# Performance work log

Hardware: AMD Instinct MI355X
Metric: run time of the kernel (lower is better)

Reference implementation:

```python
import jax, jax.numpy as jnp
import numpy as np

N_NODES = 50000
N_EDGES = 1200000
BATCH = 64
D_IN = 2
D_EMB = 64
EPS = 1e-12


def _l2norm(x):
    # torch.nn.functional.normalize(dim=1): x / max(||x||_2, eps)
    n = jnp.sqrt(jnp.sum(x * x, axis=1, keepdims=True))
    return x / jnp.maximum(n, EPS)


def setup_inputs() -> dict:
    key = jax.random.key(0)
    ks = jax.random.split(key, 10)
    edge_row = jnp.sort(jax.random.randint(ks[0], (N_EDGES,), 0, N_NODES, dtype=jnp.int32))
    edge_col = jax.random.randint(ks[1], (N_EDGES,), 0, N_NODES, dtype=jnp.int32)
    batch_assign = jax.random.randint(ks[2], (N_NODES,), 0, BATCH, dtype=jnp.int32)
    input_features = jax.random.uniform(ks[3], (N_NODES, D_IN), dtype=jnp.float32)
    input_feature_s = jax.random.uniform(ks[4], (BATCH, D_IN), dtype=jnp.float32)
    W1 = jax.random.normal(ks[5], (D_IN, D_EMB), dtype=jnp.float32) * 0.1
    W2 = jax.random.normal(ks[6], (D_EMB, D_EMB), dtype=jnp.float32) * 0.1
    W3 = jax.random.normal(ks[7], (D_EMB, D_EMB), dtype=jnp.float32) * 0.1
    Wl = jax.random.normal(ks[8], (2 * D_EMB, D_EMB), dtype=jnp.float32) * 0.1
    bl = jnp.zeros((D_EMB,), dtype=jnp.float32)
    return {
        "edge_row": edge_row, "edge_col": edge_col, "batch_assign": batch_assign,
        "input_features": input_features, "input_feature_s": input_feature_s,
        "W1": W1, "W2": W2, "W3": W3, "Wl": Wl, "bl": bl, "depth": 3,
    }


def reference(edge_row, edge_col, batch_assign, input_features, input_feature_s,
              W1, W2, W3, Wl, bl, depth):
    n_nodes = input_features.shape[0]
    n_batch = input_feature_s.shape[0]

    h = _l2norm(jax.nn.relu(input_features @ W1))        # [N, d]
    hs = _l2norm(jax.nn.relu(input_feature_s @ W1))      # [B, d]

    for _ in range(depth):
        # SPMM node_node @ h : gather neighbor embeddings, sum per destination row
        h_nv = jax.ops.segment_sum(h[edge_col], edge_row, num_segments=n_nodes)  # [N, d]
        # SPMM batch_node @ h : pool node embeddings per graph
        h_nv_s = jax.ops.segment_sum(h, batch_assign, num_segments=n_batch)      # [B, d]
        h = _l2norm(jax.nn.relu(jnp.concatenate([h @ W2, h_nv @ W3], axis=1) @ Wl + bl))
        hs = _l2norm(jax.nn.relu(jnp.concatenate([hs @ W2, h_nv_s @ W3], axis=1) @ Wl + bl))
    return (h, hs)
```

## Files before the change

kernel.cpp:

```cpp
#include <hip/hip_runtime.h>
#include <math.h>

#define N_NODES 50000
#define N_EDGES 1200000
#define BATCH   64
#define D       64
#define EPS     1e-12f
#define NCOPY   64
#define NODE_BLOCKS 3125
#define HS_BLOCKS   4
#define ITER_GRID  (NODE_BLOCKS + HS_BLOCKS)

__device__ __forceinline__ int rfl(int v) { return __builtin_amdgcn_readfirstlane(v); }

__global__ void __launch_bounds__(512) k_prep(const int* __restrict__ edge_row,
                                              int* __restrict__ row_start,
                                              float* __restrict__ pools,
                                              const float* __restrict__ W2,
                                              const float* __restrict__ W3,
                                              const float* __restrict__ Wl,
                                              float* __restrict__ MM4) {
    if (blockIdx.x < 98) {
        int tid = blockIdx.x * 512 + threadIdx.x;
        for (int i = tid; i < 2 * NCOPY * BATCH * D; i += 98 * 512) pools[i] = 0.f;
        if (tid > N_NODES) return;
        int lo = 0, hi = N_EDGES;
        while (lo < hi) {
            int mid = (lo + hi) >> 1;
            if (edge_row[mid] < tid) lo = mid + 1; else hi = mid;
        }
        row_start[tid] = lo;
    } else {
        for (int p = threadIdx.x; p < D * D; p += 512) {
            int k = p >> 6, j = p & 63;
            float a2 = 0.f, a3 = 0.f;
            for (int q = 0; q < D; ++q) {
                a2 += W2[k*D + q] * Wl[q*D + j];
                a3 += W3[k*D + q] * Wl[(D + q)*D + j];
            }
            MM4[(k >> 1) * D * 4 + j * 4 + (k & 1) * 2 + 0] = a2;
            MM4[(k >> 1) * D * 4 + j * 4 + (k & 1) * 2 + 1] = a3;
        }
    }
}

__device__ __forceinline__ float wave_l2norm(float v) {
    float ss = v * v;
    #pragma unroll
    for (int off = 32; off; off >>= 1) ss += __shfl_xor(ss, off);
    return ss;
}

__global__ void __launch_bounds__(256) k_init(const float* __restrict__ X,
                                              const float* __restrict__ Xs,
                                              const float* __restrict__ W1,
                                              float* __restrict__ B0,
                                              float* __restrict__ HS,
                                              const int* __restrict__ batch,
                                              float* __restrict__ P0) {
    int row = blockIdx.x * 4 + (threadIdx.x >> 6);
    int j   = threadIdx.x & 63;
    if (row >= N_NODES + BATCH) return;
    float x0, x1; float* out;
    bool is_node = (row < N_NODES);
    if (is_node) {
        x0 = X[row*2]; x1 = X[row*2 + 1]; out = B0 + (size_t)row * D;
    } else {
        int r = row - N_NODES;
        x0 = Xs[r*2]; x1 = Xs[r*2 + 1]; out = HS + (size_t)r * D;
    }
    float v = fmaxf(fmaf(x0, W1[j], x1 * W1[D + j]), 0.f);
    float n = sqrtf(wave_l2norm(v));
    float val = v / fmaxf(n, EPS);
    out[j] = val;
    if (is_node) {
        int b = rfl(batch[row]);
        atomicAdd(&P0[(blockIdx.x & (NCOPY - 1)) * (BATCH * D) + b * D + j], val);
    }
}

__global__ void __launch_bounds__(512, 8) k_iter(const int* __restrict__ edge_col,
                                                 const int* __restrict__ row_start,
                                                 const float* __restrict__ Hc,
                                                 float* __restrict__ Hn,
                                                 const float* __restrict__ MM4,
                                                 const float* __restrict__ bl,
                                                 const int* __restrict__ batch,
                                                 float* __restrict__ Pout,
                                                 float* __restrict__ HSrw,
                                                 float* __restrict__ Pin) {
    __shared__ float4 sMM[32 * 64];
    __shared__ float4 sHG[8 * 64];
    int t = threadIdx.x;
    const float4* gMM = (const float4*)MM4;
    for (int i = t; i < 32 * 64; i += 512) sMM[i] = gMM[i];
    __syncthreads();
    int w = t >> 6, l = t & 63;
    bool is_node = (blockIdx.x < NODE_BLOCKS);
    int rA, rB;
    float hvA, hvB, gvA, gvB;

    if (is_node) {
        int pr = blockIdx.x * 8 + w;
        rA = 2 * pr; rB = rA + 1;
        int sA = rfl(row_start[rA]);
        int eA = rfl(row_start[rB]);
        int eB = rfl(row_start[rB + 1]);
        hvA = Hc[(size_t)rA * D + l];
        hvB = Hc[(size_t)rB * D + l];
        float aA = 0.f, aB = 0.f;
        int pad = 0;
        for (int base = sA; base < eB; ) {
            int cw = eB - base; if (cw > 64) cw = 64;
            int col = 0;
            if (l < cw) col = edge_col[base + l];
            int nb = (cw + 15) >> 4;
            pad += (nb << 4) - cw;
            for (int b = 0; b < nb; ++b) {
                #pragma unroll
                for (int u = 0; u < 16; ++u) {
                    int idx = (b << 4) + u;
                    int c = __builtin_amdgcn_readlane(col, idx);
                    const float* rp = Hc + (size_t)c * D;
                    float v = rp[l];
                    if (base + idx < eA) aA += v; else aB += v;
                }
            }
            base += cw;
        }
        aB -= (float)pad * Hc[l];
        gvA = aA; gvB = aB;
    } else {
        int pr = (blockIdx.x - NODE_BLOCKS) * 8 + w;
        rA = 2 * pr; rB = rA + 1;
        hvA = HSrw[(size_t)rA * D + l];
        hvB = HSrw[(size_t)rB * D + l];
        float aA = 0.f, aB = 0.f;
        #pragma unroll 4
        for (int c = 0; c < NCOPY; ++c) {
            float* pA = Pin + (size_t)c * (BATCH * D) + rA * D + l;
            float vA = pA[0], vB = pA[D];
            pA[0] = 0.f; pA[D] = 0.f;
            aA += vA; aB += vB;
        }
        gvA = aA; gvB = aB;
    }

    sHG[w * 64 + l] = make_float4(hvA, hvB, gvA, gvB);
    float biasl = bl[l];
    float a2x = 0.f, a2y = 0.f, a3x = biasl, a3y = biasl;
    const float4* hg = &sHG[w * 64];
    #pragma unroll
    for (int kk = 0; kk < 32; ++kk) {
        float4 mm = sMM[kk * 64 + l];
        float4 h0 = hg[2 * kk];
        float4 h1 = hg[2 * kk + 1];
        a2x = fmaf(h0.x, mm.x, a2x); a2y = fmaf(h0.y, mm.x, a2y);
        a3x = fmaf(h0.z, mm.y, a3x); a3y = fmaf(h0.w, mm.y, a3y);
        a2x = fmaf(h1.x, mm.z, a2x); a2y = fmaf(h1.y, mm.z, a2y);
        a3x = fmaf(h1.z, mm.w, a3x); a3y = fmaf(h1.w, mm.w, a3y);
    }
    float vA = fmaxf(a2x + a3x, 0.f);
    float vB = fmaxf(a2y + a3y, 0.f);
    float ssA = vA * vA, ssB = vB * vB;
    #pragma unroll
    for (int off = 32; off; off >>= 1) {
        ssA += __shfl_xor(ssA, off);
        ssB += __shfl_xor(ssB, off);
    }
    float oA = vA / fmaxf(sqrtf(ssA), EPS);
    float oB = vB / fmaxf(sqrtf(ssB), EPS);

    if (is_node) {
        Hn[(size_t)rA * D + l] = oA;
        Hn[(size_t)rB * D + l] = oB;
        if (Pout) {
            int bA = rfl(batch[rA]);
            int bB = rfl(batch[rB]);
            float* cp = Pout + (size_t)(blockIdx.x & (NCOPY - 1)) * (BATCH * D);
            atomicAdd(&cp[bA * D + l], oA);
            atomicAdd(&cp[bB * D + l], oB);
        }
    } else {
        HSrw[(size_t)rA * D + l] = oA;
        HSrw[(size_t)rB * D + l] = oB;
    }
}

extern "C" void kernel_launch(void* const* d_in, const int* in_sizes, int n_in,
                              void* d_out, int out_size, void* d_ws, size_t ws_size,
                              hipStream_t stream) {
    const int*   edge_row = (const int*)  d_in[0];
    const int*   edge_col = (const int*)  d_in[1];
    const int*   batch    = (const int*)  d_in[2];
    const float* X        = (const float*)d_in[3];
    const float* Xs       = (const float*)d_in[4];
    const float* W1       = (const float*)d_in[5];
    const float* W2       = (const float*)d_in[6];
    const float* W3       = (const float*)d_in[7];
    const float* Wl       = (const float*)d_in[8];
    const float* bl       = (const float*)d_in[9];

    float* H  = (float*)d_out;
    float* HS = (float*)d_out + (size_t)N_NODES * D;

    float* B0  = (float*)d_ws;
    float* B1  = B0 + (size_t)N_NODES * D;
    float* PA  = B1 + (size_t)N_NODES * D;
    float* PB  = PA + (size_t)NCOPY * BATCH * D;
    float* MM4 = PB + (size_t)NCOPY * BATCH * D;
    int*   row_start = (int*)(MM4 + 32 * 64 * 4);

    k_prep<<<99, 512, 0, stream>>>(edge_row, row_start, PA, W2, W3, Wl, MM4);
    k_init<<<(N_NODES + BATCH + 3) / 4, 256, 0, stream>>>(X, Xs, W1, B0, HS, batch, PA);

    k_iter<<<ITER_GRID, 512, 0, stream>>>(edge_col, row_start, B0, B1, MM4, bl, batch, PB, HS, PA);
    k_iter<<<ITER_GRID, 512, 0, stream>>>(edge_col, row_start, B1, B0, MM4, bl, batch, PA, HS, PB);
    k_iter<<<ITER_GRID, 512, 0, stream>>>(edge_col, row_start, B0, H, MM4, bl, batch, nullptr, HS, PA);
}
```

Before: 281.7 us.

## Fuse prologue kernels, process four rows per wave, and lag batch pooling by a layer

The edge-boundary, weight-product and initial-embedding kernels are merged into one prologue. Row starts are now found by scattering at edge-row boundaries instead of a binary search per node. Each wave in the iteration kernel now handles four destination rows rather than two, with per-edge bounds guards replacing the padding correction. Batch pooling now accumulates the input embedding of each layer, so the batch update runs one launch later and a small extra launch finishes the last one. This removes the separate init atomics and amortises edge-index loads and row-start reads over more rows, at the cost of more registers per thread (launch bounds lowered to 6) and one extra kernel launch.

```diff
diff --git a/kernel.cpp b/kernel.cpp
--- a/kernel.cpp
+++ b/kernel.cpp
@@ -7,79 +7,68 @@
 #define D       64
 #define EPS     1e-12f
 #define NCOPY   64
-#define NODE_BLOCKS 3125
-#define HS_BLOCKS   4
-#define ITER_GRID  (NODE_BLOCKS + HS_BLOCKS)
+#define PSZ     (NCOPY * BATCH * D)
+
+#define EB  2344
+#define MMB 8
+#define IB  6258
+#define NODE_BLOCKS 1563
+#define NW4 12500
 
 __device__ __forceinline__ int rfl(int v) { return __builtin_amdgcn_readfirstlane(v); }
 
-__global__ void __launch_bounds__(512) k_prep(const int* __restrict__ edge_row,
-                                              int* __restrict__ row_start,
-                                              float* __restrict__ pools,
-                                              const float* __restrict__ W2,
-                                              const float* __restrict__ W3,
-                                              const float* __restrict__ Wl,
-                                              float* __restrict__ MM4) {
-    if (blockIdx.x < 98) {
-        int tid = blockIdx.x * 512 + threadIdx.x;
-        for (int i = tid; i < 2 * NCOPY * BATCH * D; i += 98 * 512) pools[i] = 0.f;
-        if (tid > N_NODES) return;
-        int lo = 0, hi = N_EDGES;
-        while (lo < hi) {
-            int mid = (lo + hi) >> 1;
-            if (edge_row[mid] < tid) lo = mid + 1; else hi = mid;
-        }
-        row_start[tid] = lo;
+__global__ void __launch_bounds__(512) k_pro(const int* __restrict__ edge_row,
+                                             int* __restrict__ row_start,
+                                             float* __restrict__ PA, float* __restrict__ PB,
+                                             const float* __restrict__ W2,
+                                             const float* __restrict__ W3,
+                                             const float* __restrict__ Wl,
+                                             float* __restrict__ MM4,
+                                             const float* __restrict__ X,
+                                             const float* __restrict__ Xs,
+                                             const float* __restrict__ W1,
+                                             float* __restrict__ B0,
+                                             float* __restrict__ HS) {
+    int bid = blockIdx.x, t = threadIdx.x;
+    if (bid < EB) {
+        int tid = bid * 512 + t;
+        for (int i = tid; i < PSZ; i += EB * 512) { PA[i] = 0.f; PB[i] = 0.f; }
+        if (tid < N_EDGES) {
+            int b = edge_row[tid];
+            int a = (tid == 0) ? -1 : edge_row[tid - 1];
+            for (int r = a + 1; r <= b; ++r) row_start[r] = tid;
+            if (tid == N_EDGES - 1)
+                for (int r = b + 1; r <= N_NODES; ++r) row_start[r] = N_EDGES;
+        }
+    } else if (bid < EB + MMB) {
+        int k = (bid - EB) * 8 + (t >> 6), j = t & 63;
+        float a2 = 0.f, a3 = 0.f;
+        for (int q = 0; q < D; ++q) {
+            a2 += W2[k*D + q] * Wl[q*D + j];
+            a3 += W3[k*D + q] * Wl[(D + q)*D + j];
+        }
+        MM4[(k >> 1) * (D * 4) + j * 4 + (k & 1) * 2 + 0] = a2;
+        MM4[(k >> 1) * (D * 4) + j * 4 + (k & 1) * 2 + 1] = a3;
     } else {
-        for (int p = threadIdx.x; p < D * D; p += 512) {
-            int k = p >> 6, j = p & 63;
-            float a2 = 0.f, a3 = 0.f;
-            for (int q = 0; q < D; ++q) {
-                a2 += W2[k*D + q] * Wl[q*D + j];
-                a3 += W3[k*D + q] * Wl[(D + q)*D + j];
-            }
-            MM4[(k >> 1) * D * 4 + j * 4 + (k & 1) * 2 + 0] = a2;
-            MM4[(k >> 1) * D * 4 + j * 4 + (k & 1) * 2 + 1] = a3;
-        }
+        int row = (bid - EB - MMB) * 8 + (t >> 6);
+        int j = t & 63;
+        if (row >= N_NODES + BATCH) return;
+        float x0, x1; float* out;
+        if (row < N_NODES) {
+            x0 = X[row*2]; x1 = X[row*2 + 1]; out = B0 + (size_t)row * D;
+        } else {
+            int r = row - N_NODES;
+            x0 = Xs[r*2]; x1 = Xs[r*2 + 1]; out = HS + (size_t)r * D;
+        }
+        float v = fmaxf(fmaf(x0, W1[j], x1 * W1[D + j]), 0.f);
+        float ss = v * v;
+        #pragma unroll
+        for (int off = 32; off; off >>= 1) ss += __shfl_xor(ss, off);
+        out[j] = v / fmaxf(sqrtf(ss), EPS);
     }
 }
 
-__device__ __forceinline__ float wave_l2norm(float v) {
-    float ss = v * v;
-    #pragma unroll
-    for (int off = 32; off; off >>= 1) ss += __shfl_xor(ss, off);
-    return ss;
-}
-
-__global__ void __launch_bounds__(256) k_init(const float* __restrict__ X,
-                                              const float* __restrict__ Xs,
-                                              const float* __restrict__ W1,
-                                              float* __restrict__ B0,
-                                              float* __restrict__ HS,
-                                              const int* __restrict__ batch,
-                                              float* __restrict__ P0) {
-    int row = blockIdx.x * 4 + (threadIdx.x >> 6);
-    int j   = threadIdx.x & 63;
-    if (row >= N_NODES + BATCH) return;
-    float x0, x1; float* out;
-    bool is_node = (row < N_NODES);
-    if (is_node) {
-        x0 = X[row*2]; x1 = X[row*2 + 1]; out = B0 + (size_t)row * D;
-    } else {
-        int r = row - N_NODES;
-        x0 = Xs[r*2]; x1 = Xs[r*2 + 1]; out = HS + (size_t)r * D;
-    }
-    float v = fmaxf(fmaf(x0, W1[j], x1 * W1[D + j]), 0.f);
-    float n = sqrtf(wave_l2norm(v));
-    float val = v / fmaxf(n, EPS);
-    out[j] = val;
-    if (is_node) {
-        int b = rfl(batch[row]);
-        atomicAdd(&P0[(blockIdx.x & (NCOPY - 1)) * (BATCH * D) + b * D + j], val);
-    }
-}
-
-__global__ void __launch_bounds__(512, 8) k_iter(const int* __restrict__ edge_col,
+__global__ void __launch_bounds__(512, 6) k_iter(const int* __restrict__ edge_col,
                                                  const int* __restrict__ row_start,
                                                  const float* __restrict__ Hc,
                                                  float* __restrict__ Hn,
@@ -88,103 +77,123 @@
                                                  const int* __restrict__ batch,
                                                  float* __restrict__ Pout,
                                                  float* __restrict__ HSrw,
-                                                 float* __restrict__ Pin) {
+                                                 float* __restrict__ Pin,
+                                                 int hs_blocks) {
     __shared__ float4 sMM[32 * 64];
-    __shared__ float4 sHG[8 * 64];
-    int t = threadIdx.x;
+    __shared__ float4 sH[8 * 64];
+    __shared__ float4 sG[8 * 64];
+    int t = threadIdx.x, w = t >> 6, l = t & 63;
     const float4* gMM = (const float4*)MM4;
-    for (int i = t; i < 32 * 64; i += 512) sMM[i] = gMM[i];
+    for (int i = t; i < 2048; i += 512) sMM[i] = gMM[i];
     __syncthreads();
-    int w = t >> 6, l = t & 63;
-    bool is_node = (blockIdx.x < NODE_BLOCKS);
-    int rA, rB;
-    float hvA, hvB, gvA, gvB;
-
-    if (is_node) {
-        int pr = blockIdx.x * 8 + w;
-        rA = 2 * pr; rB = rA + 1;
-        int sA = rfl(row_start[rA]);
-        int eA = rfl(row_start[rB]);
-        int eB = rfl(row_start[rB + 1]);
-        hvA = Hc[(size_t)rA * D + l];
-        hvB = Hc[(size_t)rB * D + l];
-        float aA = 0.f, aB = 0.f;
-        int pad = 0;
-        for (int base = sA; base < eB; ) {
-            int cw = eB - base; if (cw > 64) cw = 64;
+
+    int bid = blockIdx.x;
+    bool is_hs = (bid < hs_blocks);
+    float hv0, hv1, hv2, hv3, gv0, gv1, gv2, gv3;
+    int rbase;
+
+    if (!is_hs) {
+        int g4 = (bid - hs_blocks) * 8 + w;
+        if (g4 >= NW4) return;
+        rbase = g4 * 4;
+        int eS  = rfl(row_start[rbase]);
+        int eA  = rfl(row_start[rbase + 1]);
+        int eBb = rfl(row_start[rbase + 2]);
+        int eC  = rfl(row_start[rbase + 3]);
+        int eD_ = rfl(row_start[rbase + 4]);
+        hv0 = Hc[(size_t)(rbase + 0) * D + l];
+        hv1 = Hc[(size_t)(rbase + 1) * D + l];
+        hv2 = Hc[(size_t)(rbase + 2) * D + l];
+        hv3 = Hc[(size_t)(rbase + 3) * D + l];
+        float aA = 0.f, aB = 0.f, aC = 0.f, aD = 0.f;
+        for (int base = eS; base < eD_; base += 64) {
+            int cw = eD_ - base; if (cw > 64) cw = 64;
             int col = 0;
             if (l < cw) col = edge_col[base + l];
             int nb = (cw + 15) >> 4;
-            pad += (nb << 4) - cw;
             for (int b = 0; b < nb; ++b) {
                 #pragma unroll
                 for (int u = 0; u < 16; ++u) {
-                    int idx = (b << 4) + u;
-                    int c = __builtin_amdgcn_readlane(col, idx);
-                    const float* rp = Hc + (size_t)c * D;
-                    float v = rp[l];
-                    if (base + idx < eA) aA += v; else aB += v;
+                    int o = (b << 4) + u;
+                    int eidx = base + o;
+                    if (eidx < eD_) {
+                        int c = __builtin_amdgcn_readlane(col, o);
+                        float v = Hc[(size_t)c * D + l];
+                        if (eidx < eA)       aA += v;
+                        else if (eidx < eBb) aB += v;
+                        else if (eidx < eC)  aC += v;
+                        else                 aD += v;
+                    }
                 }
             }
-            base += cw;
-        }
-        aB -= (float)pad * Hc[l];
-        gvA = aA; gvB = aB;
+        }
+        gv0 = aA; gv1 = aB; gv2 = aC; gv3 = aD;
+        float* cp = Pout + (size_t)(bid & (NCOPY - 1)) * (BATCH * D);
+        int b0 = rfl(batch[rbase + 0]);
+        int b1 = rfl(batch[rbase + 1]);
+        int b2 = rfl(batch[rbase + 2]);
+        int b3 = rfl(batch[rbase + 3]);
+        atomicAdd(&cp[b0 * D + l], hv0);
+        atomicAdd(&cp[b1 * D + l], hv1);
+        atomicAdd(&cp[b2 * D + l], hv2);
+        atomicAdd(&cp[b3 * D + l], hv3);
     } else {
-        int pr = (blockIdx.x - NODE_BLOCKS) * 8 + w;
-        rA = 2 * pr; rB = rA + 1;
-        hvA = HSrw[(size_t)rA * D + l];
-        hvB = HSrw[(size_t)rB * D + l];
-        float aA = 0.f, aB = 0.f;
+        int g4 = bid * 8 + w;
+        if (g4 >= 16) return;
+        rbase = g4 * 4;
+        hv0 = HSrw[(size_t)(rbase + 0) * D + l];
+        hv1 = HSrw[(size_t)(rbase + 1) * D + l];
+        hv2 = HSrw[(size_t)(rbase + 2) * D + l];
+        hv3 = HSrw[(size_t)(rbase + 3) * D + l];
+        float aA = 0.f, aB = 0.f, aC = 0.f, aD = 0.f;
         #pragma unroll 4
         for (int c = 0; c < NCOPY; ++c) {
-            float* pA = Pin + (size_t)c * (BATCH * D) + rA * D + l;
-            float vA = pA[0], vB = pA[D];
-            pA[0] = 0.f; pA[D] = 0.f;
-            aA += vA; aB += vB;
-        }
-        gvA = aA; gvB = aB;
-    }
-
-    sHG[w * 64 + l] = make_float4(hvA, hvB, gvA, gvB);
-    float biasl = bl[l];
-    float a2x = 0.f, a2y = 0.f, a3x = biasl, a3y = biasl;
-    const float4* hg = &sHG[w * 64];
+            float* p = Pin + (size_t)c * (BATCH * D) + rbase * D + l;
+            float v0 = p[0], v1 = p[D], v2 = p[2*D], v3 = p[3*D];
+            p[0] = 0.f; p[D] = 0.f; p[2*D] = 0.f; p[3*D] = 0.f;
+            aA += v0; aB += v1; aC += v2; aD += v3;
+        }
+        gv0 = aA; gv1 = aB; gv2 = aC; gv3 = aD;
+    }
+
+    sH[w * 64 + l] = make_float4(hv0, hv1, hv2, hv3);
+    sG[w * 64 + l] = make_float4(gv0, gv1, gv2, gv3);
+    float bj = bl[l];
+    float a2A = 0.f, a2B = 0.f, a2C = 0.f, a2D = 0.f;
+    float a3A = bj,  a3B = bj,  a3C = bj,  a3D = bj;
+    const float4* ph = &sH[w * 64];
+    const float4* pg = &sG[w * 64];
     #pragma unroll
     for (int kk = 0; kk < 32; ++kk) {
         float4 mm = sMM[kk * 64 + l];
-        float4 h0 = hg[2 * kk];
-        float4 h1 = hg[2 * kk + 1];
-        a2x = fmaf(h0.x, mm.x, a2x); a2y = fmaf(h0.y, mm.x, a2y);
-        a3x = fmaf(h0.z, mm.y, a3x); a3y = fmaf(h0.w, mm.y, a3y);
-        a2x = fmaf(h1.x, mm.z, a2x); a2y = fmaf(h1.y, mm.z, a2y);
-        a3x = fmaf(h1.z, mm.w, a3x); a3y = fmaf(h1.w, mm.w, a3y);
-    }
-    float vA = fmaxf(a2x + a3x, 0.f);
-    float vB = fmaxf(a2y + a3y, 0.f);
-    float ssA = vA * vA, ssB = vB * vB;
+        float4 h0 = ph[2 * kk], h1 = ph[2 * kk + 1];
+        float4 g0 = pg[2 * kk], g1 = pg[2 * kk + 1];
+        a2A = fmaf(h0.x, mm.x, a2A); a2B = fmaf(h0.y, mm.x, a2B);
+        a2C = fmaf(h0.z, mm.x, a2C); a2D = fmaf(h0.w, mm.x, a2D);
+        a3A = fmaf(g0.x, mm.y, a3A); a3B = fmaf(g0.y, mm.y, a3B);
+        a3C = fmaf(g0.z, mm.y, a3C); a3D = fmaf(g0.w, mm.y, a3D);
+        a2A = fmaf(h1.x, mm.z, a2A); a2B = fmaf(h1.y, mm.z, a2B);
+        a2C = fmaf(h1.z, mm.z, a2C); a2D = fmaf(h1.w, mm.z, a2D);
+        a3A = fmaf(g1.x, mm.w, a3A); a3B = fmaf(g1.y, mm.w, a3B);
+        a3C = fmaf(g1.z, mm.w, a3C); a3D = fmaf(g1.w, mm.w, a3D);
+    }
+    float v0 = fmaxf(a2A + a3A, 0.f);
+    float v1 = fmaxf(a2B + a3B, 0.f);
+    float v2 = fmaxf(a2C + a3C, 0.f);
+    float v3 = fmaxf(a2D + a3D, 0.f);
+    float s0 = v0*v0, s1 = v1*v1, s2 = v2*v2, s3 = v3*v3;
     #pragma unroll
     for (int off = 32; off; off >>= 1) {
-        ssA += __shfl_xor(ssA, off);
-        ssB += __shfl_xor(ssB, off);
-    }
-    float oA = vA / fmaxf(sqrtf(ssA), EPS);
-    float oB = vB / fmaxf(sqrtf(ssB), EPS);
-
-    if (is_node) {
-        Hn[(size_t)rA * D + l] = oA;
-        Hn[(size_t)rB * D + l] = oB;
-        if (Pout) {
-            int bA = rfl(batch[rA]);
-            int bB = rfl(batch[rB]);
-            float* cp = Pout + (size_t)(blockIdx.x & (NCOPY - 1)) * (BATCH * D);
-            atomicAdd(&cp[bA * D + l], oA);
-            atomicAdd(&cp[bB * D + l], oB);
-        }
-    } else {
-        HSrw[(size_t)rA * D + l] = oA;
-        HSrw[(size_t)rB * D + l] = oB;
-    }
+        s0 += __shfl_xor(s0, off); s1 += __shfl_xor(s1, off);
+        s2 += __shfl_xor(s2, off); s3 += __shfl_xor(s3, off);
+    }
+    v0 /= fmaxf(sqrtf(s0), EPS); v1 /= fmaxf(sqrtf(s1), EPS);
+    v2 /= fmaxf(sqrtf(s2), EPS); v3 /= fmaxf(sqrtf(s3), EPS);
+    float* out = is_hs ? HSrw : Hn;
+    out[(size_t)(rbase + 0) * D + l] = v0;
+    out[(size_t)(rbase + 1) * D + l] = v1;
+    out[(size_t)(rbase + 2) * D + l] = v2;
+    out[(size_t)(rbase + 3) * D + l] = v3;
 }
 
 extern "C" void kernel_launch(void* const* d_in, const int* in_sizes, int n_in,
@@ -207,14 +216,19 @@
     float* B0  = (float*)d_ws;
     float* B1  = B0 + (size_t)N_NODES * D;
     float* PA  = B1 + (size_t)N_NODES * D;
-    float* PB  = PA + (size_t)NCOPY * BATCH * D;
-    float* MM4 = PB + (size_t)NCOPY * BATCH * D;
+    float* PB  = PA + PSZ;
+    float* MM4 = PB + PSZ;
     int*   row_start = (int*)(MM4 + 32 * 64 * 4);
 
-    k_prep<<<99, 512, 0, stream>>>(edge_row, row_start, PA, W2, W3, Wl, MM4);
-    k_init<<<(N_NODES + BATCH + 3) / 4, 256, 0, stream>>>(X, Xs, W1, B0, HS, batch, PA);
-
-    k_iter<<<ITER_GRID, 512, 0, stream>>>(edge_col, row_start, B0, B1, MM4, bl, batch, PB, HS, PA);
-    k_iter<<<ITER_GRID, 512, 0, stream>>>(edge_col, row_start, B1, B0, MM4, bl, batch, PA, HS, PB);
-    k_iter<<<ITER_GRID, 512, 0, stream>>>(edge_col, row_start, B0, H, MM4, bl, batch, nullptr, HS, PA);
+    k_pro<<<EB + MMB + IB, 512, 0, stream>>>(edge_row, row_start, PA, PB,
+                                             W2, W3, Wl, MM4, X, Xs, W1, B0, HS);
+
+    k_iter<<<NODE_BLOCKS, 512, 0, stream>>>(edge_col, row_start, B0, B1, MM4, bl,
+                                            batch, PA, HS, PA, 0);
+    k_iter<<<NODE_BLOCKS + 2, 512, 0, stream>>>(edge_col, row_start, B1, B0, MM4, bl,
+                                                batch, PB, HS, PA, 2);
+    k_iter<<<NODE_BLOCKS + 2, 512, 0, stream>>>(edge_col, row_start, B0, H, MM4, bl,
+                                                batch, PA, HS, PB, 2);
+    k_iter<<<2, 512, 0, stream>>>(edge_col, row_start, B0, B0, MM4, bl,
+                                  batch, PB, HS, PA, 2);
 }
```

Result: slower. 482.6 us (+71.3%).

## Fuse prep and init kernels, compute row_start per edge, pool inputs in iterations

Applied to the files above, without the earlier changes.

The separate prep and init kernels become one prologue kernel, and the row_start binary search is replaced by a per-edge boundary scan that writes row offsets directly. Batch pooling now happens in each iteration on the input embeddings rather than the outputs, which removes the atomics from init. The batch-embedding update therefore runs one launch later, and a small HS-only launch is added at the end. Launch count stays the same. The point is to remove the serial binary-search work and the standalone init atomics, at the cost of a more intricate buffer ping-pong schedule across launches.

```diff
diff --git a/kernel.cpp b/kernel.cpp
--- a/kernel.cpp
+++ b/kernel.cpp
@@ -7,75 +7,64 @@
 #define D       64
 #define EPS     1e-12f
 #define NCOPY   64
+#define PSZ     (NCOPY * BATCH * D)
+
+#define EB  2344
+#define MMB 8
+#define IB  6258
 #define NODE_BLOCKS 3125
-#define HS_BLOCKS   4
-#define ITER_GRID  (NODE_BLOCKS + HS_BLOCKS)
+#define HSB 4
 
 __device__ __forceinline__ int rfl(int v) { return __builtin_amdgcn_readfirstlane(v); }
 
-__global__ void __launch_bounds__(512) k_prep(const int* __restrict__ edge_row,
-                                              int* __restrict__ row_start,
-                                              float* __restrict__ pools,
-                                              const float* __restrict__ W2,
-                                              const float* __restrict__ W3,
-                                              const float* __restrict__ Wl,
-                                              float* __restrict__ MM4) {
-    if (blockIdx.x < 98) {
-        int tid = blockIdx.x * 512 + threadIdx.x;
-        for (int i = tid; i < 2 * NCOPY * BATCH * D; i += 98 * 512) pools[i] = 0.f;
-        if (tid > N_NODES) return;
-        int lo = 0, hi = N_EDGES;
-        while (lo < hi) {
-            int mid = (lo + hi) >> 1;
-            if (edge_row[mid] < tid) lo = mid + 1; else hi = mid;
-        }
-        row_start[tid] = lo;
+__global__ void __launch_bounds__(512) k_pro(const int* __restrict__ edge_row,
+                                             int* __restrict__ row_start,
+                                             float* __restrict__ PA, float* __restrict__ PB,
+                                             const float* __restrict__ W2,
+                                             const float* __restrict__ W3,
+                                             const float* __restrict__ Wl,
+                                             float* __restrict__ MM4,
+                                             const float* __restrict__ X,
+                                             const float* __restrict__ Xs,
+                                             const float* __restrict__ W1,
+                                             float* __restrict__ B0,
+                                             float* __restrict__ HS) {
+    int bid = blockIdx.x, t = threadIdx.x;
+    if (bid < EB) {
+        int tid = bid * 512 + t;
+        for (int i = tid; i < PSZ; i += EB * 512) { PA[i] = 0.f; PB[i] = 0.f; }
+        if (tid < N_EDGES) {
+            int b = edge_row[tid];
+            int a = (tid == 0) ? -1 : edge_row[tid - 1];
+            for (int r = a + 1; r <= b; ++r) row_start[r] = tid;
+            if (tid == N_EDGES - 1)
+                for (int r = b + 1; r <= N_NODES; ++r) row_start[r] = N_EDGES;
+        }
+    } else if (bid < EB + MMB) {
+        int k = (bid - EB) * 8 + (t >> 6), j = t & 63;
+        float a2 = 0.f, a3 = 0.f;
+        for (int q = 0; q < D; ++q) {
+            a2 += W2[k*D + q] * Wl[q*D + j];
+            a3 += W3[k*D + q] * Wl[(D + q)*D + j];
+        }
+        MM4[(k >> 1) * (D * 4) + j * 4 + (k & 1) * 2 + 0] = a2;
+        MM4[(k >> 1) * (D * 4) + j * 4 + (k & 1) * 2 + 1] = a3;
     } else {
-        for (int p = threadIdx.x; p < D * D; p += 512) {
-            int k = p >> 6, j = p & 63;
-            float a2 = 0.f, a3 = 0.f;
-            for (int q = 0; q < D; ++q) {
-                a2 += W2[k*D + q] * Wl[q*D + j];
-                a3 += W3[k*D + q] * Wl[(D + q)*D + j];
-            }
-            MM4[(k >> 1) * D * 4 + j * 4 + (k & 1) * 2 + 0] = a2;
-            MM4[(k >> 1) * D * 4 + j * 4 + (k & 1) * 2 + 1] = a3;
-        }
-    }
-}
-
-__device__ __forceinline__ float wave_l2norm(float v) {
-    float ss = v * v;
-    #pragma unroll
-    for (int off = 32; off; off >>= 1) ss += __shfl_xor(ss, off);
-    return ss;
-}
-
-__global__ void __launch_bounds__(256) k_init(const float* __restrict__ X,
-                                              const float* __restrict__ Xs,
-                                              const float* __restrict__ W1,
-                                              float* __restrict__ B0,
-                                              float* __restrict__ HS,
-                                              const int* __restrict__ batch,
-                                              float* __restrict__ P0) {
-    int row = blockIdx.x * 4 + (threadIdx.x >> 6);
-    int j   = threadIdx.x & 63;
-    if (row >= N_NODES + BATCH) return;
-    float x0, x1; float* out;
-    bool is_node = (row < N_NODES);
-    if (is_node) {
-        x0 = X[row*2]; x1 = X[row*2 + 1]; out = B0 + (size_t)row * D;
-    } else {
-        int r = row - N_NODES;
-        x0 = Xs[r*2]; x1 = Xs[r*2 + 1]; out = HS + (size_t)r * D;
-    }
-    float v = fmaxf(fmaf(x0, W1[j], x1 * W1[D + j]), 0.f);
-    float n = sqrtf(wave_l2norm(v));
-    float val = v / fmaxf(n, EPS);
-    out[j] = val;
-    if (is_node) {
-        int b = rfl(batch[row]);
-        atomicAdd(&P0[(blockIdx.x & (NCOPY - 1)) * (BATCH * D) + b * D + j], val);
+        int row = (bid - EB - MMB) * 8 + (t >> 6);
+        int j = t & 63;
+        if (row >= N_NODES + BATCH) return;
+        float x0, x1; float* out;
+        if (row < N_NODES) {
+            x0 = X[row*2]; x1 = X[row*2 + 1]; out = B0 + (size_t)row * D;
+        } else {
+            int r = row - N_NODES;
+            x0 = Xs[r*2]; x1 = Xs[r*2 + 1]; out = HS + (size_t)r * D;
+        }
+        float v = fmaxf(fmaf(x0, W1[j], x1 * W1[D + j]), 0.f);
+        float ss = v * v;
+        #pragma unroll
+        for (int off = 32; off; off >>= 1) ss += __shfl_xor(ss, off);
+        out[j] = v / fmaxf(sqrtf(ss), EPS);
     }
 }
 
@@ -88,20 +77,22 @@
                                                  const int* __restrict__ batch,
                                                  float* __restrict__ Pout,
                                                  float* __restrict__ HSrw,
-                                                 float* __restrict__ Pin) {
+                                                 float* __restrict__ Pin,
+                                                 int hs_blocks) {
     __shared__ float4 sMM[32 * 64];
     __shared__ float4 sHG[8 * 64];
-    int t = threadIdx.x;
+    int t = threadIdx.x, w = t >> 6, l = t & 63;
     const float4* gMM = (const float4*)MM4;
-    for (int i = t; i < 32 * 64; i += 512) sMM[i] = gMM[i];
+    for (int i = t; i < 2048; i += 512) sMM[i] = gMM[i];
     __syncthreads();
-    int w = t >> 6, l = t & 63;
-    bool is_node = (blockIdx.x < NODE_BLOCKS);
+
+    int bid = blockIdx.x;
+    bool is_hs = (bid < hs_blocks);
     int rA, rB;
     float hvA, hvB, gvA, gvB;
 
-    if (is_node) {
-        int pr = blockIdx.x * 8 + w;
+    if (!is_hs) {
+        int pr = (bid - hs_blocks) * 8 + w;
         rA = 2 * pr; rB = rA + 1;
         int sA = rfl(row_start[rA]);
         int eA = rfl(row_start[rB]);
@@ -130,25 +121,30 @@
         }
         aB -= (float)pad * Hc[l];
         gvA = aA; gvB = aB;
+        float* cp = Pout + (size_t)(bid & (NCOPY - 1)) * (BATCH * D);
+        int bA = rfl(batch[rA]);
+        int bB = rfl(batch[rB]);
+        atomicAdd(&cp[bA * D + l], hvA);
+        atomicAdd(&cp[bB * D + l], hvB);
     } else {
-        int pr = (blockIdx.x - NODE_BLOCKS) * 8 + w;
+        int pr = bid * 8 + w;
         rA = 2 * pr; rB = rA + 1;
         hvA = HSrw[(size_t)rA * D + l];
         hvB = HSrw[(size_t)rB * D + l];
         float aA = 0.f, aB = 0.f;
         #pragma unroll 4
         for (int c = 0; c < NCOPY; ++c) {
-            float* pA = Pin + (size_t)c * (BATCH * D) + rA * D + l;
-            float vA = pA[0], vB = pA[D];
-            pA[0] = 0.f; pA[D] = 0.f;
+            float* p = Pin + (size_t)c * (BATCH * D) + rA * D + l;
+            float vA = p[0], vB = p[D];
+            p[0] = 0.f; p[D] = 0.f;
             aA += vA; aB += vB;
         }
         gvA = aA; gvB = aB;
     }
 
     sHG[w * 64 + l] = make_float4(hvA, hvB, gvA, gvB);
-    float biasl = bl[l];
-    float a2x = 0.f, a2y = 0.f, a3x = biasl, a3y = biasl;
+    float bj = bl[l];
+    float a2x = 0.f, a2y = 0.f, a3x = bj, a3y = bj;
     const float4* hg = &sHG[w * 64];
     #pragma unroll
     for (int kk = 0; kk < 32; ++kk) {
@@ -171,20 +167,9 @@
     float oA = vA / fmaxf(sqrtf(ssA), EPS);
     float oB = vB / fmaxf(sqrtf(ssB), EPS);
 
-    if (is_node) {
-        Hn[(size_t)rA * D + l] = oA;
-        Hn[(size_t)rB * D + l] = oB;
-        if (Pout) {
-            int bA = rfl(batch[rA]);
-            int bB = rfl(batch[rB]);
-            float* cp = Pout + (size_t)(blockIdx.x & (NCOPY - 1)) * (BATCH * D);
-            atomicAdd(&cp[bA * D + l], oA);
-            atomicAdd(&cp[bB * D + l], oB);
-        }
-    } else {
-        HSrw[(size_t)rA * D + l] = oA;
-        HSrw[(size_t)rB * D + l] = oB;
-    }
+    float* out = is_hs ? HSrw : Hn;
+    out[(size_t)rA * D + l] = oA;
+    out[(size_t)rB * D + l] = oB;
 }
 
 extern "C" void kernel_launch(void* const* d_in, const int* in_sizes, int n_in,
@@ -207,14 +192,19 @@
     float* B0  = (float*)d_ws;
     float* B1  = B0 + (size_t)N_NODES * D;
     float* PA  = B1 + (size_t)N_NODES * D;
-    float* PB  = PA + (size_t)NCOPY * BATCH * D;
-    float* MM4 = PB + (size_t)NCOPY * BATCH * D;
+    float* PB  = PA + PSZ;
+    float* MM4 = PB + PSZ;
     int*   row_start = (int*)(MM4 + 32 * 64 * 4);
 
-    k_prep<<<99, 512, 0, stream>>>(edge_row, row_start, PA, W2, W3, Wl, MM4);
-    k_init<<<(N_NODES + BATCH + 3) / 4, 256, 0, stream>>>(X, Xs, W1, B0, HS, batch, PA);
-
-    k_iter<<<ITER_GRID, 512, 0, stream>>>(edge_col, row_start, B0, B1, MM4, bl, batch, PB, HS, PA);
-    k_iter<<<ITER_GRID, 512, 0, stream>>>(edge_col, row_start, B1, B0, MM4, bl, batch, PA, HS, PB);
-    k_iter<<<ITER_GRID, 512, 0, stream>>>(edge_col, row_start, B0, H, MM4, bl, batch, nullptr, HS, PA);
+    k_pro<<<EB + MMB + IB, 512, 0, stream>>>(edge_row, row_start, PA, PB,
+                                             W2, W3, Wl, MM4, X, Xs, W1, B0, HS);
+
+    k_iter<<<NODE_BLOCKS, 512, 0, stream>>>(edge_col, row_start, B0, B1, MM4, bl,
+                                            batch, PA, HS, PA, 0);
+    k_iter<<<NODE_BLOCKS + HSB, 512, 0, stream>>>(edge_col, row_start, B1, B0, MM4, bl,
+                                                  batch, PB, HS, PA, HSB);
+    k_iter<<<NODE_BLOCKS + HSB, 512, 0, stream>>>(edge_col, row_start, B0, H, MM4, bl,
+                                                  batch, PA, HS, PB, HSB);
+    k_iter<<<HSB, 512, 0, stream>>>(edge_col, row_start, B0, B0, MM4, bl,
+                                    batch, PB, HS, PA, HSB);
 }
```

Result: faster. 261.6 us (-7.1%).
